# Kernel optimization log

Hardware: AMD Instinct MI355X
Metric: run time of the kernel (lower is better)

The kernel has to match this reference:

```python
import jax, jax.numpy as jnp
import numpy as np

ACTION_SCALE = 0.01
LOG_STD_MIN, LOG_STD_MAX = -20.0, 2.0


def setup_inputs() -> dict:
    key = jax.random.key(0)
    k1, k2, k3 = jax.random.split(key, 3)
    B, N, D = 8, 1024, 128
    kv = jax.random.normal(k1, (B, N, 4 * D), dtype=jnp.float32)
    positions = jax.random.normal(k2, (B, N, 3), dtype=jnp.float32)
    eps = jax.random.normal(k3, (B, N, 3), dtype=jnp.float32)  # standard-normal sample for rsample
    return {"kv": kv, "positions": positions, "eps": eps}


def reference(kv, positions, eps):
    # Split Atomwise output into mean/std key-value embeddings: each [B, N, D]
    k_mu, v_mu, k_sigma, v_sigma = jnp.split(kv, 4, axis=-1)

    # Low-rank attention-like pairwise scores: [B, N, N]
    rel_shifts_mean = jnp.einsum("bid,bjd->bij", k_mu, v_mu)
    rel_shifts_log_std = jnp.einsum("bid,bjd->bij", k_sigma, v_sigma)

    # All-pairs unit displacement vectors: [B, N, N, 3]
    P = positions[:, :, None, :] - positions[:, None, :, :]
    norm = jnp.linalg.norm(P, axis=-1) + 1e-8
    P = P / norm[..., None]

    # Weighted sum over the j axis (torch dim=-2): [B, N, 3]
    actions_mean = jnp.einsum("bijc,bij->bic", P, rel_shifts_mean)
    actions_log_std = jnp.clip(
        jnp.einsum("bijc,bij->bic", P, rel_shifts_log_std), LOG_STD_MIN, LOG_STD_MAX
    )
    actions_std = jnp.exp(actions_log_std)

    # TanhNormal rsample (training branch) with externally supplied noise eps
    pre_tanh = actions_mean + actions_std * eps
    actions = jnp.tanh(pre_tanh)

    # Normal log-prob minus tanh log-det-Jacobian
    normal_lp = (
        -0.5 * ((pre_tanh - actions_mean) / actions_std) ** 2
        - actions_log_std
        - 0.5 * jnp.log(2.0 * jnp.pi)
    )
    log_det = (
        2.0 * jnp.log(2.0)
        + jax.nn.log_sigmoid(2.0 * pre_tanh)
        + jax.nn.log_sigmoid(-2.0 * pre_tanh)
    )
    log_prob = jnp.sum(normal_lp - log_det, axis=(1, 2))[:, None]  # [B, 1]

    actions = actions * ACTION_SCALE
    # change-of-variables correction for the action_scale factor
    n_dims = pre_tanh.shape[1] * pre_tanh.shape[2]
    log_prob = log_prob - n_dims * jnp.log(ACTION_SCALE)
    return actions, log_prob
```

## Files before the change

kernel.cpp:

```cpp
#include <hip/hip_runtime.h>
#include <math.h>


#define NTOK 1024
#define LPCONST 14147.0828114f

typedef __bf16 bf16x8 __attribute__((ext_vector_type(8)));
typedef float f32x4 __attribute__((ext_vector_type(4)));
typedef unsigned short ushort8v __attribute__((ext_vector_type(8)));
#define MFMA(a, b, c) __builtin_amdgcn_mfma_f32_16x16x32_bf16(a, b, c, 0, 0, 0)

__device__ __forceinline__ unsigned short to_bf16(float x) {
    return (unsigned short)((__float_as_uint(x) + 0x8000u) >> 16);
}

__device__ __forceinline__ ushort8v pack8(float4 a, float4 b) {
    ushort8v u;
    u[0] = to_bf16(a.x); u[1] = to_bf16(a.y); u[2] = to_bf16(a.z); u[3] = to_bf16(a.w);
    u[4] = to_bf16(b.x); u[5] = to_bf16(b.y); u[6] = to_bf16(b.z); u[7] = to_bf16(b.w);
    return u;
}

__device__ __forceinline__ bf16x8 cvt8(float4 a, float4 b) {
    return __builtin_bit_cast(bf16x8, pack8(a, b));
}

__global__ __launch_bounds__(512) void actor_kernel(
    const float* __restrict__ kv, const float* __restrict__ pos,
    float* __restrict__ partial, float* __restrict__ out)
{
    const int t = threadIdx.x;
    const int w = t >> 6;
    const int lane = t & 63;
    const int q = lane >> 4;
    const int r16 = lane & 15;
    const int b   = blockIdx.x & 7;
    const int jh  = (blockIdx.x >> 3) & 3;
    const int ibx = blockIdx.x >> 5;
    const int i0 = ibx * 64;

    if (blockIdx.x < 8 && t == 0) out[8 * NTOK * 3 + blockIdx.x] = LPCONST;

    const float* kvb  = kv + (size_t)b * NTOK * 512;
    const float* posb = pos + (size_t)b * NTOK * 3;

    __shared__ __align__(16) unsigned short sK[16384];
    __shared__ __align__(16) float spos[NTOK * 3];
    __shared__ float wacc[8 * 64 * 6];

    {
        const int ri = t >> 3;
        const int cg = t & 7;
        const float* gp = kvb + (size_t)(i0 + ri) * 512 + cg * 16;
        const float4 m0 = *(const float4*)(gp);
        const float4 m1 = *(const float4*)(gp + 4);
        const float4 m2 = *(const float4*)(gp + 8);
        const float4 m3 = *(const float4*)(gp + 12);
        const float4 s0 = *(const float4*)(gp + 256);
        const float4 s1 = *(const float4*)(gp + 260);
        const float4 s2 = *(const float4*)(gp + 264);
        const float4 s3 = *(const float4*)(gp + 268);
        unsigned short* dp = sK + (ri >> 4) * 4096 + (cg >> 1) * 1024
                           + ((cg & 1) * 32 + (ri & 15)) * 8;
        *(ushort8v*)(dp)       = pack8(m0, m1);
        *(ushort8v*)(dp + 128) = pack8(m2, m3);
        *(ushort8v*)(dp + 512) = pack8(s0, s1);
        *(ushort8v*)(dp + 640) = pack8(s2, s3);
    }
    for (int u = t; u < 768; u += 512)
        *(float4*)&spos[u * 4] = *(const float4*)&posb[u * 4];
    __syncthreads();

    float pix[4], piy[4], piz[4];
    #pragma unroll
    for (int tile = 0; tile < 4; ++tile) {
        pix[tile] = spos[(i0 + tile * 16 + r16) * 3 + 0];
        piy[tile] = spos[(i0 + tile * 16 + r16) * 3 + 1];
        piz[tile] = spos[(i0 + tile * 16 + r16) * 3 + 2];
    }

    float am[4][3] = {};
    float al[4][3] = {};

    const int jtile0 = jh * 16 + w * 2;
    const float* vrow = kvb + (size_t)(jtile0 * 16 + r16) * 512 + 128 + q * 8;
    const int klofs = lane * 8;

    #pragma unroll
    for (int jt = 0; jt < 2; ++jt) {
        const float* vp = vrow + (size_t)jt * 16 * 512;
        f32x4 accm[4], accs[4];
        #pragma unroll
        for (int tile = 0; tile < 4; ++tile) {
            accm[tile] = (f32x4){0.f, 0.f, 0.f, 0.f};
            accs[tile] = (f32x4){0.f, 0.f, 0.f, 0.f};
        }
        #pragma unroll
        for (int kc = 0; kc < 4; ++kc) {
            const float4 vm0 = *(const float4*)(vp + kc * 32);
            const float4 vm1 = *(const float4*)(vp + kc * 32 + 4);
            const bf16x8 Vm = cvt8(vm0, vm1);
            const float4 vs0 = *(const float4*)(vp + kc * 32 + 256);
            const float4 vs1 = *(const float4*)(vp + kc * 32 + 260);
            const bf16x8 Vs = cvt8(vs0, vs1);
            #pragma unroll
            for (int tile = 0; tile < 4; ++tile) {
                const bf16x8 Km = *(const bf16x8*)&sK[tile * 4096 + kc * 1024 + klofs];
                const bf16x8 Ks = *(const bf16x8*)&sK[tile * 4096 + kc * 1024 + 512 + klofs];
                accm[tile] = MFMA(Vm, Km, accm[tile]);
                accs[tile] = MFMA(Vs, Ks, accs[tile]);
            }
        }
        const int jbase = (jtile0 + jt) * 16 + q * 4;
        #pragma unroll
        for (int reg = 0; reg < 4; ++reg) {
            const float* pj = &spos[(jbase + reg) * 3];
            const float pjx = pj[0], pjy = pj[1], pjz = pj[2];
            #pragma unroll
            for (int tile = 0; tile < 4; ++tile) {
                const float dx = pix[tile] - pjx;
                const float dy = piy[tile] - pjy;
                const float dz = piz[tile] - pjz;
                const float d2 = dx * dx + dy * dy + dz * dz;
                const float inv = d2 > 0.f ? rsqrtf(d2) : 0.f;
                const float wm = accm[tile][reg] * inv;
                const float ws = accs[tile][reg] * inv;
                am[tile][0] = fmaf(dx, wm, am[tile][0]);
                am[tile][1] = fmaf(dy, wm, am[tile][1]);
                am[tile][2] = fmaf(dz, wm, am[tile][2]);
                al[tile][0] = fmaf(dx, ws, al[tile][0]);
                al[tile][1] = fmaf(dy, ws, al[tile][1]);
                al[tile][2] = fmaf(dz, ws, al[tile][2]);
            }
        }
    }

    #pragma unroll
    for (int tile = 0; tile < 4; ++tile)
        #pragma unroll
        for (int c = 0; c < 3; ++c) {
            float vm = am[tile][c], vl = al[tile][c];
            vm += __shfl_xor(vm, 16, 64); vm += __shfl_xor(vm, 32, 64);
            vl += __shfl_xor(vl, 16, 64); vl += __shfl_xor(vl, 32, 64);
            am[tile][c] = vm; al[tile][c] = vl;
        }

    if (lane < 16) {
        #pragma unroll
        for (int tile = 0; tile < 4; ++tile) {
            float* p = wacc + (w * 64 + tile * 16 + r16) * 6;
            p[0] = am[tile][0]; p[1] = am[tile][1]; p[2] = am[tile][2];
            p[3] = al[tile][0]; p[4] = al[tile][1]; p[5] = al[tile][2];
        }
    }
    __syncthreads();
    if (t < 384) {
        float v = 0.f;
        #pragma unroll
        for (int ww = 0; ww < 8; ++ww) v += wacc[ww * 384 + t];
        const int row = t / 6, c = t - row * 6;
        partial[((size_t)((jh * 8 + b) * NTOK) + i0 + row) * 6 + c] = v;
    }
}

__global__ __launch_bounds__(64) void actor_tail_kernel(
    const float* __restrict__ partial, const float* __restrict__ eps,
    float* __restrict__ out)
{
    const int b = blockIdx.x >> 4;
    const int i = (blockIdx.x & 15) * 64 + threadIdx.x;
    const int gi = b * NTOK + i;

    float am[3] = {}, al[3] = {};
    #pragma unroll
    for (int jh = 0; jh < 4; ++jh) {
        const float* p = partial + (((size_t)jh * 8 + b) * NTOK + i) * 6;
        const float2 v0 = *(const float2*)(p);
        const float2 v1 = *(const float2*)(p + 2);
        const float2 v2 = *(const float2*)(p + 4);
        am[0] += v0.x; am[1] += v0.y; am[2] += v1.x;
        al[0] += v1.y; al[1] += v2.x; al[2] += v2.y;
    }

    float lp = 0.f;
    #pragma unroll
    for (int c = 0; c < 3; ++c) {
        const float als = fminf(fmaxf(al[c], -20.f), 2.f);
        const float sd = __expf(als);
        const float e = eps[gi * 3 + c];
        const float pre = fmaf(sd, e, am[c]);
        const float a2 = 2.f * fabsf(pre);
        const float E = __expf(-a2);
        const float th = (1.f - E) / (1.f + E);
        out[gi * 3 + c] = copysignf(th, pre) * 0.01f;
        lp += fmaf(-0.5f * e, e, -als) - 2.3052328944f + a2 + 2.f * __logf(1.f + E);
    }

    #pragma unroll
    for (int m = 1; m < 64; m <<= 1) lp += __shfl_xor(lp, m, 64);
    if (threadIdx.x == 0) atomicAdd(out + NTOK * 8 * 3 + b, lp);
}

extern "C" void kernel_launch(void* const* d_in, const int* in_sizes, int n_in,
                              void* d_out, int out_size, void* d_ws, size_t ws_size,
                              hipStream_t stream) {
    const float* kv = (const float*)d_in[0];
    const float* pos = (const float*)d_in[1];
    const float* eps = (const float*)d_in[2];
    float* out = (float*)d_out;
    float* partial = (float*)d_ws;

    actor_kernel<<<dim3(512), 512, 0, stream>>>(kv, pos, partial, out);
    actor_tail_kernel<<<dim3(128), 64, 0, stream>>>(partial, eps, out);
}
```

Baseline: 93.62 us.

## Precompute bf16 MFMA-fragment layout for V operands in a prepass kernel

Adds a prepass kernel that converts the v_mu/v_sigma columns of kv to bf16 once and stores them in MFMA fragment order in workspace. The main kernel then loads each V fragment as a single 16-byte read instead of reading fp32 rows and converting them. Without this, each V row is re-read and re-converted by the 16 i-blocks that use it. The cost is an extra kernel launch plus a full pass over the V half of kv, and the initialization of the log-prob constant moves into the prepass.

```diff
diff --git a/kernel.cpp b/kernel.cpp
--- a/kernel.cpp
+++ b/kernel.cpp
@@ -21,13 +21,34 @@
     return u;
 }
 
-__device__ __forceinline__ bf16x8 cvt8(float4 a, float4 b) {
-    return __builtin_bit_cast(bf16x8, pack8(a, b));
+__global__ __launch_bounds__(256) void prepass_kernel(
+    const float* __restrict__ kv, unsigned short* __restrict__ frag,
+    float* __restrict__ out)
+{
+    const int t = blockIdx.x * 256 + threadIdx.x;
+    if (t < 8) out[8 * NTOK * 3 + t] = LPCONST;
+
+    const int lane = t & 63;
+    const int kc   = (t >> 6) & 3;
+    const int tile = (t >> 8) & 63;
+    const int b    = (t >> 14) & 7;
+
+    const int row = tile * 16 + (lane & 15);
+    const int kof = kc * 32 + (lane >> 4) * 8;
+    const float* gp = kv + ((size_t)b * NTOK + row) * 512 + 128 + kof;
+    const float4 m0 = *(const float4*)gp;
+    const float4 m1 = *(const float4*)(gp + 4);
+    const float4 s0 = *(const float4*)(gp + 256);
+    const float4 s1 = *(const float4*)(gp + 260);
+
+    unsigned short* cp = frag + (size_t)(b * 64 + tile) * 4096 + kc * 1024 + lane * 8;
+    *(ushort8v*)(cp + 0)   = pack8(m0, m1);
+    *(ushort8v*)(cp + 512) = pack8(s0, s1);
 }
 
 __global__ __launch_bounds__(512) void actor_kernel(
-    const float* __restrict__ kv, const float* __restrict__ pos,
-    float* __restrict__ partial, float* __restrict__ out)
+    const float* __restrict__ kv, const unsigned short* __restrict__ fragV,
+    const float* __restrict__ pos, float* __restrict__ partial)
 {
     const int t = threadIdx.x;
     const int w = t >> 6;
@@ -38,8 +59,6 @@
     const int jh  = (blockIdx.x >> 3) & 3;
     const int ibx = blockIdx.x >> 5;
     const int i0 = ibx * 64;
-
-    if (blockIdx.x < 8 && t == 0) out[8 * NTOK * 3 + blockIdx.x] = LPCONST;
 
     const float* kvb  = kv + (size_t)b * NTOK * 512;
     const float* posb = pos + (size_t)b * NTOK * 3;
@@ -83,12 +102,13 @@
     float al[4][3] = {};
 
     const int jtile0 = jh * 16 + w * 2;
-    const float* vrow = kvb + (size_t)(jtile0 * 16 + r16) * 512 + 128 + q * 8;
+    const unsigned short* vbase =
+        fragV + (size_t)(b * 64 + jtile0) * 4096 + lane * 8;
     const int klofs = lane * 8;
 
     #pragma unroll
     for (int jt = 0; jt < 2; ++jt) {
-        const float* vp = vrow + (size_t)jt * 16 * 512;
+        const unsigned short* vp = vbase + jt * 4096;
         f32x4 accm[4], accs[4];
         #pragma unroll
         for (int tile = 0; tile < 4; ++tile) {
@@ -97,12 +117,8 @@
         }
         #pragma unroll
         for (int kc = 0; kc < 4; ++kc) {
-            const float4 vm0 = *(const float4*)(vp + kc * 32);
-            const float4 vm1 = *(const float4*)(vp + kc * 32 + 4);
-            const bf16x8 Vm = cvt8(vm0, vm1);
-            const float4 vs0 = *(const float4*)(vp + kc * 32 + 256);
-            const float4 vs1 = *(const float4*)(vp + kc * 32 + 260);
-            const bf16x8 Vs = cvt8(vs0, vs1);
+            const bf16x8 Vm = *(const bf16x8*)(vp + kc * 1024);
+            const bf16x8 Vs = *(const bf16x8*)(vp + kc * 1024 + 512);
             #pragma unroll
             for (int tile = 0; tile < 4; ++tile) {
                 const bf16x8 Km = *(const bf16x8*)&sK[tile * 4096 + kc * 1024 + klofs];
@@ -208,8 +224,10 @@
     const float* pos = (const float*)d_in[1];
     const float* eps = (const float*)d_in[2];
     float* out = (float*)d_out;
-    float* partial = (float*)d_ws;
-
-    actor_kernel<<<dim3(512), 512, 0, stream>>>(kv, pos, partial, out);
+    unsigned short* fragV = (unsigned short*)d_ws;
+    float* partial = (float*)((char*)d_ws + 4194304);
+
+    prepass_kernel<<<dim3(512), 256, 0, stream>>>(kv, fragV, out);
+    actor_kernel<<<dim3(512), 512, 0, stream>>>(kv, fragV, pos, partial);
     actor_tail_kernel<<<dim3(128), 64, 0, stream>>>(partial, eps, out);
 }
```

New measurement: 85.52 us. -8.7%, faster.
